# Kernel tuning notes

Hardware: AMD Instinct MI355X
Metric: run time of the kernel (lower is better)

Reference implementation:

```python
import jax, jax.numpy as jnp
import numpy as np

N_NODES = 50000
N_EDGES = 800000
IN_CH = 64
HID = 128
OUT_CH = 1
NUM_LAYERS = 3
NUM_TIMESTEPS = 3
EDGE_DIM = 25
NUM_GRAPHS = 1024
NEG = 0.01  # leaky_relu negative slope (torch default & GATConv arg)


def leaky(v):
    return jnp.where(v >= 0, v, NEG * v)


def seg_softmax(a, idx, n):
    # PyG softmax: exp(a - max_per_segment) / (sum_per_segment + 1e-16)
    m = jax.ops.segment_max(a, idx, num_segments=n)
    m = jnp.where(jnp.isfinite(m), m, 0.0)  # guard empty segments
    e = jnp.exp(a - m[idx])
    s = jax.ops.segment_sum(e, idx, num_segments=n)
    return e / (s[idx] + 1e-16)


def gru(inp, h, Wih, Whh, bih, bhh):
    gi = inp @ Wih.T + bih
    gh = h @ Whh.T + bhh
    ir, iz, inn = jnp.split(gi, 3, axis=-1)
    hr, hz, hn = jnp.split(gh, 3, axis=-1)
    r = jax.nn.sigmoid(ir + hr)
    z = jax.nn.sigmoid(iz + hz)
    n = jnp.tanh(inn + r * hn)
    return (1.0 - z) * n + z * h


def setup_inputs() -> dict:
    key = jax.random.key(0)
    ks = iter(jax.random.split(key, 40))

    def nrm(shape, s=0.05):
        return jax.random.normal(next(ks), shape, dtype=jnp.float32) * s

    L = NUM_LAYERS - 1
    H3 = 3 * HID
    inp = dict(
        x=jax.random.normal(next(ks), (N_NODES, IN_CH), dtype=jnp.float32),
        edge_index=jax.random.randint(next(ks), (2, N_EDGES), 0, N_NODES),
        batch=jnp.sort(jax.random.randint(next(ks), (N_NODES,), 0, NUM_GRAPHS)),
        W1=nrm((HID, IN_CH)), b1=jnp.zeros((HID,), jnp.float32),
        Wg1=nrm((HID, HID + EDGE_DIM)), att_l=nrm((HID,)), att_r=nrm((HID,)),
        Wg2=nrm((HID, HID)), bg=jnp.zeros((HID,), jnp.float32),
        Wih0=nrm((H3, HID)), Whh0=nrm((H3, HID)),
        bih0=jnp.zeros((H3,), jnp.float32), bhh0=jnp.zeros((H3,), jnp.float32),
        Wa=nrm((L, HID, HID)), att_src_a=nrm((L, HID)), att_dst_a=nrm((L, HID)),
        ba=jnp.zeros((L, HID), jnp.float32),
        Wih_a=nrm((L, H3, HID)), Whh_a=nrm((L, H3, HID)),
        bih_a=jnp.zeros((L, H3), jnp.float32), bhh_a=jnp.zeros((L, H3), jnp.float32),
        Wm=nrm((HID, HID)), att_src_m=nrm((HID,)), att_dst_m=nrm((HID,)),
        bm=jnp.zeros((HID,), jnp.float32),
        Wih_m=nrm((H3, HID)), Whh_m=nrm((H3, HID)),
        bih_m=jnp.zeros((H3,), jnp.float32), bhh_m=jnp.zeros((H3,), jnp.float32),
        W2=nrm((OUT_CH, HID)), b2=jnp.zeros((OUT_CH,), jnp.float32),
    )
    return inp


def reference(x, edge_index, batch, W1, b1, Wg1, att_l, att_r, Wg2, bg,
              Wih0, Whh0, bih0, bhh0, Wa, att_src_a, att_dst_a, ba,
              Wih_a, Whh_a, bih_a, bhh_a, Wm, att_src_m, att_dst_m, bm,
              Wih_m, Whh_m, bih_m, bhh_m, W2, b2):
    N = x.shape[0]
    E = edge_index.shape[1]
    src, dst = edge_index[0], edge_index[1]  # j -> i, aggregate at i=dst
    edge_attr = jnp.ones((E, EDGE_DIM), dtype=x.dtype)  # built inside original forward

    x = leaky(x @ W1.T + b1)

    # GATEConv: edge-feature-aware attention, sum aggregation
    xe = leaky(jnp.concatenate([x[src], edge_attr], axis=-1) @ Wg1.T)  # [E, H]
    a = seg_softmax(leaky(xe @ att_l + (x @ att_r)[dst]), dst, N)
    msg = (x[src] @ Wg2.T) * a[:, None]
    h = jax.nn.elu(jax.ops.segment_sum(msg, dst, num_segments=N) + bg)
    x = jax.nn.relu(gru(h, x, Wih0, Whh0, bih0, bhh0))

    # (num_layers - 1) GATConv + GRU atom updates
    for l in range(NUM_LAYERS - 1):
        xt = x @ Wa[l].T
        a = seg_softmax(leaky((xt @ att_src_a[l])[src] + (xt @ att_dst_a[l])[dst]), dst, N)
        h = jax.nn.elu(jax.ops.segment_sum(xt[src] * a[:, None], dst, num_segments=N) + ba[l])
        x = jax.nn.relu(gru(h, x, Wih_a[l], Whh_a[l], bih_a[l], bhh_a[l]))

    # attentive readout: bipartite GATConv node->molecule over num_timesteps
    out = jax.nn.relu(jax.ops.segment_sum(x, batch, num_segments=NUM_GRAPHS))
    xt = x @ Wm.T                 # shared lin for src (fixed across timesteps)
    a_src = xt @ att_src_m        # [N]
    for _ in range(NUM_TIMESTEPS):
        ot = out @ Wm.T           # shared lin for dst
        a = seg_softmax(leaky(a_src + (ot @ att_dst_m)[batch]), batch, NUM_GRAPHS)
        h = jax.nn.elu(jax.ops.segment_sum(xt * a[:, None], batch, num_segments=NUM_GRAPHS) + bm)
        out = jax.nn.relu(gru(h, out, Wih_m, Whh_m, bih_m, bhh_m))

    return out @ W2.T + b2
```

## Files before the change

kernel.cpp:

```cpp
#include <hip/hip_runtime.h>
#include <math.h>

#define NN 50000
#define NE 800000
#define NG 1024
#define HID 128

typedef __attribute__((ext_vector_type(8))) short short8;
typedef __attribute__((ext_vector_type(4))) unsigned short ushort4v;
typedef __attribute__((ext_vector_type(4))) float f32x4;

__device__ __forceinline__ float leakyf(float v){ return v >= 0.f ? v : 0.01f*v; }
__device__ __forceinline__ float frcp(float x){ return __builtin_amdgcn_rcpf(x); }
__device__ __forceinline__ float fsigm(float v){ return frcp(1.f + __expf(-v)); }
__device__ __forceinline__ float ftanh(float v){ return 1.f - 2.f*frcp(1.f + __expf(2.f*v)); }
__device__ __forceinline__ float eluf(float v){ return v > 0.f ? v : __expf(v) - 1.f; }
__device__ __forceinline__ unsigned short bf16rne(float f){
  union { float f; unsigned u; } v; v.f = f;
  return (unsigned short)((v.u + 0x7FFFu + ((v.u >> 16) & 1u)) >> 16);
}
__device__ __forceinline__ float bf2f(unsigned short h){
  union { unsigned u; float f; } v; v.u = ((unsigned)h) << 16; return v.f;
}
__device__ __forceinline__ short8 cvt8(const float* a){
  short8 r;
#pragma unroll
  for (int j=0;j<8;j++) r[j] = (short)bf16rne(a[j]);
  return r;
}

__global__ __launch_bounds__(256)
void pack_all(const float* W1, const float* Wg1, const float* Wg2, const float* Wa,
              const float* Wm, const float* Wih0, const float* Whh0,
              const float* Wih_a, const float* Whh_a,
              unsigned short* __restrict__ dst)
{
  int m = (int)blockIdx.y;
  int t = (int)blockIdx.x*4 + ((int)threadIdx.x>>6);
  int l = (int)threadIdx.x & 63;
  const float* src; int stride=128, M=128, K=128; size_t doff;
  switch(m){
    case 0:  src=W1;    stride=64;  K=64;  doff=0;      break;
    case 1:  src=Wg1;   stride=153;        doff=8192;   break;
    case 2:  src=Wg2;                      doff=24576;  break;
    case 3:  src=Wa;                       doff=40960;  break;
    case 4:  src=Wa+16384;                 doff=57344;  break;
    case 5:  src=Wm;                       doff=73728;  break;
    case 6:  src=Wih0;  M=384;             doff=90112;  break;
    case 7:  src=Whh0;  M=384;             doff=139264; break;
    case 8:  src=Wih_a; M=384;             doff=188416; break;
    case 9:  src=Whh_a; M=384;             doff=237568; break;
    case 10: src=Wih_a+49152; M=384;       doff=286720; break;
    default: src=Whh_a+49152; M=384;       doff=335872; break;
  }
  int tk = K/32;
  if (t >= (M/16)*tk) return;
  int ct = t / tk, kc = t % tk;
  int row = ct*16 + (l&15);
  int col = kc*32 + ((l>>4)<<3);
  unsigned short o[8];
#pragma unroll
  for (int j=0;j<8;j++) o[j] = bf16rne(src[(size_t)row*stride + col + j]);
  ushort4v* d = (ushort4v*)(dst + doff + (((size_t)t*64 + l)<<3));
  ushort4v d0; d0.x=o[0]; d0.y=o[1]; d0.z=o[2]; d0.w=o[3];
  ushort4v d1; d1.x=o[4]; d1.y=o[5]; d1.z=o[6]; d1.w=o[7];
  d[0]=d0; d[1]=d1;
}

__global__ void pack_t4(const float* __restrict__ Wi, const float* __restrict__ Wh,
                        unsigned short* __restrict__ Wit, unsigned short* __restrict__ Wht)
{
  int q  = (int)blockIdx.x;
  int cg = (int)threadIdx.x + (int)blockIdx.y*128;
  ushort4v a, b;
#pragma unroll
  for (int j=0;j<4;j++){
    a[j] = bf16rne(Wi[(size_t)cg*128 + q*4 + j]);
    b[j] = bf16rne(Wh[(size_t)cg*128 + q*4 + j]);
  }
  *(ushort4v*)&Wit[((size_t)q*384 + cg)*4] = a;
  *(ushort4v*)&Wht[((size_t)q*384 + cg)*4] = b;
}

__global__ __launch_bounds__(256)
void gemm_f32(const float* __restrict__ A, const unsigned short* __restrict__ Wp,
              const float* __restrict__ bias, float* __restrict__ Cf,
              unsigned short* __restrict__ Cb, int rows, int act)
{
  constexpr int K = 64, KC = 2;
  const int tid=(int)threadIdx.x, w=tid>>6, l=tid&63;
  const int fr=l&15, fq=l>>4;
  const int rt=w>>1, ch=w&1;
  const int bn = (int)blockIdx.x*32;
  const int ar = bn + rt*16 + fr;
  f32x4 acc[4];
#pragma unroll
  for (int j=0;j<4;j++) acc[j] = (f32x4){0.f,0.f,0.f,0.f};
#pragma unroll
  for (int kc=0;kc<KC;kc++){
    float a8[8];
    if (ar < rows){
      *(float4*)&a8[0] = *(const float4*)(A + (size_t)ar*K + kc*32 + fq*8);
      *(float4*)&a8[4] = *(const float4*)(A + (size_t)ar*K + kc*32 + fq*8 + 4);
    } else {
#pragma unroll
      for (int j=0;j<8;j++) a8[j]=0.f;
    }
    short8 fa = cvt8(a8);
#pragma unroll
    for (int j=0;j<4;j++){
      const short8 bfr = *(const short8*)(Wp + ((((size_t)(ch*4+j)*KC + kc)*64 + l)<<3));
      acc[j] = __builtin_amdgcn_mfma_f32_16x16x32_bf16(fa, bfr, acc[j], 0, 0, 0);
    }
  }
#pragma unroll
  for (int j=0;j<4;j++){
    int c = ch*64 + j*16 + fr;
    float bv = bias ? bias[c] : 0.f;
#pragma unroll
    for (int r4=0;r4<4;r4++){
      float o = acc[j][r4] + bv;
      if (act) o = leakyf(o);
      int r = bn + rt*16 + fq*4 + r4;
      if (r < rows){
        Cf[(size_t)r*HID + c] = o;
        Cb[(size_t)r*HID + c] = bf16rne(o);
      }
    }
  }
}

__global__ __launch_bounds__(256)
void gemm_b16(const unsigned short* __restrict__ Ab, const unsigned short* __restrict__ Wp,
              const float* __restrict__ bias, unsigned short* __restrict__ Cb,
              const float* __restrict__ v1, const float* __restrict__ v2,
              float* __restrict__ s1, float* __restrict__ s2, int rows, int act)
{
  __shared__ float sd1[2][32];
  __shared__ float sd2[2][32];
  constexpr int KC = 4;
  const int tid=(int)threadIdx.x, w=tid>>6, l=tid&63;
  const int fr=l&15, fq=l>>4;
  const int rt=w>>1, ch=w&1;
  const int bn = (int)blockIdx.x*32;
  const int ar = bn + rt*16 + fr;
  f32x4 acc[4];
#pragma unroll
  for (int j=0;j<4;j++) acc[j] = (f32x4){0.f,0.f,0.f,0.f};
#pragma unroll
  for (int kc=0;kc<KC;kc++){
    short8 fa;
    if (ar < rows) fa = *(const short8*)(Ab + (size_t)ar*HID + kc*32 + fq*8);
    else { short8 z = {0,0,0,0,0,0,0,0}; fa = z; }
#pragma unroll
    for (int j=0;j<4;j++){
      const short8 bfr = *(const short8*)(Wp + ((((size_t)(ch*4+j)*KC + kc)*64 + l)<<3));
      acc[j] = __builtin_amdgcn_mfma_f32_16x16x32_bf16(fa, bfr, acc[j], 0, 0, 0);
    }
  }
  float dp1[4]={0.f,0.f,0.f,0.f}, dp2[4]={0.f,0.f,0.f,0.f};
#pragma unroll
  for (int j=0;j<4;j++){
    int c = ch*64 + j*16 + fr;
    float bv = bias ? bias[c] : 0.f;
    float w1 = v1 ? v1[c] : 0.f;
    float w2 = v2 ? v2[c] : 0.f;
#pragma unroll
    for (int r4=0;r4<4;r4++){
      float o = acc[j][r4] + bv;
      if (act) o = leakyf(o);
      dp1[r4] += o*w1; dp2[r4] += o*w2;
      int r = bn + rt*16 + fq*4 + r4;
      if (r < rows && Cb) Cb[(size_t)r*HID + c] = bf16rne(o);
    }
  }
  if (v1){
#pragma unroll
    for (int r4=0;r4<4;r4++){
#pragma unroll
      for (int m=1;m<16;m<<=1){ dp1[r4] += __shfl_xor(dp1[r4], m); dp2[r4] += __shfl_xor(dp2[r4], m); }
    }
    if (fr==0){
#pragma unroll
      for (int r4=0;r4<4;r4++){
        sd1[ch][rt*16 + fq*4 + r4] = dp1[r4];
        sd2[ch][rt*16 + fq*4 + r4] = dp2[r4];
      }
    }
    __syncthreads();
    if (tid < 32){
      int r = bn + tid;
      if (r < rows) s1[r] = sd1[0][tid] + sd1[1][tid];
    } else if (v2 && tid < 64){
      int r = bn + tid - 32;
      if (r < rows) s2[r] = sd2[0][tid-32] + sd2[1][tid-32];
    }
  }
}

__global__ __launch_bounds__(256)
void gemm_gate(const unsigned short* __restrict__ Ab,
               const unsigned short* __restrict__ W1p, const unsigned short* __restrict__ W2p,
               const float* __restrict__ cg, const float* __restrict__ attl,
               const float* __restrict__ attr,
               unsigned short* __restrict__ Cb,
               float* __restrict__ s1, float* __restrict__ s2, int rows)
{
  __shared__ float sd1[2][32];
  constexpr int KC = 4;
  const int tid=(int)threadIdx.x, w=tid>>6, l=tid&63;
  const int fr=l&15, fq=l>>4;
  const int rt=w>>1, ch=w&1;
  const int bn = (int)blockIdx.x*32;
  const int ar = bn + rt*16 + fr;
  f32x4 acc1[4], acc2[4];
#pragma unroll
  for (int j=0;j<4;j++){ acc1[j]=(f32x4){0,0,0,0}; acc2[j]=(f32x4){0,0,0,0}; }
  float pa = 0.f;
#pragma unroll
  for (int kc=0;kc<KC;kc++){
    short8 fa;
    if (ar < rows) fa = *(const short8*)(Ab + (size_t)ar*HID + kc*32 + fq*8);
    else { short8 z = {0,0,0,0,0,0,0,0}; fa = z; }
    if (ch==0){
      float4 t0 = *(const float4*)(attr + kc*32 + fq*8);
      float4 t1 = *(const float4*)(attr + kc*32 + fq*8 + 4);
      pa += bf2f((unsigned short)fa[0])*t0.x + bf2f((unsigned short)fa[1])*t0.y
          + bf2f((unsigned short)fa[2])*t0.z + bf2f((unsigned short)fa[3])*t0.w
          + bf2f((unsigned short)fa[4])*t1.x + bf2f((unsigned short)fa[5])*t1.y
          + bf2f((unsigned short)fa[6])*t1.z + bf2f((unsigned short)fa[7])*t1.w;
    }
#pragma unroll
    for (int j=0;j<4;j++){
      size_t wo = ((((size_t)(ch*4+j)*KC + kc)*64 + l)<<3);
      acc1[j] = __builtin_amdgcn_mfma_f32_16x16x32_bf16(fa, *(const short8*)(W1p + wo), acc1[j], 0, 0, 0);
      acc2[j] = __builtin_amdgcn_mfma_f32_16x16x32_bf16(fa, *(const short8*)(W2p + wo), acc2[j], 0, 0, 0);
    }
  }
  float dp1[4]={0.f,0.f,0.f,0.f};
#pragma unroll
  for (int j=0;j<4;j++){
    int c = ch*64 + j*16 + fr;
    float bv = cg[c];
    float w1 = attl[c];
#pragma unroll
    for (int r4=0;r4<4;r4++){
      float o1 = leakyf(acc1[j][r4] + bv);
      dp1[r4] += o1*w1;
      int r = bn + rt*16 + fq*4 + r4;
      if (r < rows) Cb[(size_t)r*HID + c] = bf16rne(acc2[j][r4]);
    }
  }
#pragma unroll
  for (int r4=0;r4<4;r4++){
#pragma unroll
    for (int m=1;m<16;m<<=1) dp1[r4] += __shfl_xor(dp1[r4], m);
  }
  if (fr==0){
#pragma unroll
    for (int r4=0;r4<4;r4++) sd1[ch][rt*16 + fq*4 + r4] = dp1[r4];
  }
  __syncthreads();
  if (tid < 32){
    int r = bn + tid;
    if (r < rows) s1[r] = sd1[0][tid] + sd1[1][tid];
  }
  if (ch==0){
    pa += __shfl_xor(pa, 16); pa += __shfl_xor(pa, 32);
    if (fq==0){
      int r = bn + rt*16 + fr;
      if (r < rows) s2[r] = pa;
    }
  }
}

#define GRU_TPB 4
__global__ __launch_bounds__(512, 2)
void fused_gru(const unsigned short* __restrict__ Ahb, const unsigned short* __restrict__ Axb,
               const float* __restrict__ Axf,
               const unsigned short* __restrict__ Wi, const unsigned short* __restrict__ Wh,
               const float* __restrict__ bih, const float* __restrict__ bhh,
               float* __restrict__ outf, unsigned short* __restrict__ outb, int tiles)
{
  const int tid=(int)threadIdx.x, w=tid>>6, l=tid&63;
  const int fr=l&15, fq=l>>4;
  short8 wi_r[3][4], wh_r[3][4];
#pragma unroll
  for (int g=0;g<3;g++)
#pragma unroll
    for (int kc=0;kc<4;kc++){
      size_t o = ((((size_t)(g*8 + w)*4 + kc)*64 + l)<<3);
      wi_r[g][kc] = *(const short8*)(Wi + o);
      wh_r[g][kc] = *(const short8*)(Wh + o);
    }
  const int c0 = w*16 + fr;
  float bi0=bih[c0], bi1=bih[c0+128], bi2=bih[c0+256];
  float bh0=bhh[c0], bh1=bhh[c0+128], bh2=bhh[c0+256];

  int rt = (int)blockIdx.x*GRU_TPB;
  int rt_end = min(rt + GRU_TPB, tiles);
  if (rt >= tiles) return;
  short8 fa[4], fx[4];
  float hv[4];
  {
    const int arow = rt*16 + fr;
#pragma unroll
    for (int kc=0;kc<4;kc++){
      fa[kc] = *(const short8*)(Ahb + (size_t)arow*HID + kc*32 + fq*8);
      fx[kc] = *(const short8*)(Axb + (size_t)arow*HID + kc*32 + fq*8);
    }
#pragma unroll
    for (int r4=0;r4<4;r4++) hv[r4] = Axf[(size_t)(rt*16 + fq*4 + r4)*HID + c0];
  }
  for (; rt < rt_end; rt++){
    short8 nfa[4], nfx[4];
    float nhv[4];
    if (rt+1 < rt_end){
      const int arow = (rt+1)*16 + fr;
#pragma unroll
      for (int kc=0;kc<4;kc++){
        nfa[kc] = *(const short8*)(Ahb + (size_t)arow*HID + kc*32 + fq*8);
        nfx[kc] = *(const short8*)(Axb + (size_t)arow*HID + kc*32 + fq*8);
      }
#pragma unroll
      for (int r4=0;r4<4;r4++) nhv[r4] = Axf[(size_t)((rt+1)*16 + fq*4 + r4)*HID + c0];
    }
    f32x4 ai0={0,0,0,0}, ai1={0,0,0,0}, ai2={0,0,0,0};
    f32x4 ah0={0,0,0,0}, ah1={0,0,0,0}, ah2={0,0,0,0};
#pragma unroll
    for (int kc=0;kc<4;kc++){
      ai0 = __builtin_amdgcn_mfma_f32_16x16x32_bf16(fa[kc], wi_r[0][kc], ai0, 0, 0, 0);
      ai1 = __builtin_amdgcn_mfma_f32_16x16x32_bf16(fa[kc], wi_r[1][kc], ai1, 0, 0, 0);
      ai2 = __builtin_amdgcn_mfma_f32_16x16x32_bf16(fa[kc], wi_r[2][kc], ai2, 0, 0, 0);
      ah0 = __builtin_amdgcn_mfma_f32_16x16x32_bf16(fx[kc], wh_r[0][kc], ah0, 0, 0, 0);
      ah1 = __builtin_amdgcn_mfma_f32_16x16x32_bf16(fx[kc], wh_r[1][kc], ah1, 0, 0, 0);
      ah2 = __builtin_amdgcn_mfma_f32_16x16x32_bf16(fx[kc], wh_r[2][kc], ah2, 0, 0, 0);
    }
#pragma unroll
    for (int r4=0;r4<4;r4++){
      int row = rt*16 + fq*4 + r4;
      float rr = fsigm(ai0[r4] + bi0 + ah0[r4] + bh0);
      float zz = fsigm(ai1[r4] + bi1 + ah1[r4] + bh1);
      float nn = ftanh(ai2[r4] + bi2 + rr*(ah2[r4] + bh2));
      float o = fmaxf((1.f - zz)*nn + zz*hv[r4], 0.f);
      outf[(size_t)row*HID + c0] = o;
      outb[(size_t)row*HID + c0] = bf16rne(o);
    }
#pragma unroll
    for (int kc=0;kc<4;kc++){ fa[kc]=nfa[kc]; fx[kc]=nfx[kc]; }
#pragma unroll
    for (int r4=0;r4<4;r4++) hv[r4]=nhv[r4];
  }
}

__global__ void colvec(const float* __restrict__ W, const float* __restrict__ v,
                       float* __restrict__ out)
{
  int k = (int)threadIdx.x;
  float s = 0.f;
  for (int j=0;j<HID;j++) s += W[j*HID+k]*v[j];
  out[k] = s;
}

__global__ void prep_cg(const float* __restrict__ Wg1, float* __restrict__ cg){
  int j = (int)threadIdx.x;
  float s = 0.f;
  for (int k=128;k<153;k++) s += Wg1[j*153+k];
  cg[j] = s;
}

__global__ void count_kernel(const int* __restrict__ idx, int* __restrict__ cnt, int n){
  int i = (int)(blockIdx.x*blockDim.x + threadIdx.x);
  if (i < n) atomicAdd(&cnt[idx[i]], 1);
}

__global__ __launch_bounds__(1024)
void scan_blocks(const int* __restrict__ cnt, int* __restrict__ off,
                 int* __restrict__ tot, int n)
{
  __shared__ int buf[1024];
  int i = (int)(blockIdx.x*1024 + threadIdx.x);
  int v = (i<n)? cnt[i] : 0;
  buf[threadIdx.x] = v;
  __syncthreads();
  for (int s=1;s<1024;s<<=1){
    int t = ((int)threadIdx.x >= s) ? buf[threadIdx.x - s] : 0;
    __syncthreads();
    buf[threadIdx.x] += t;
    __syncthreads();
  }
  if (i<n) off[i] = buf[threadIdx.x] - v;
  if (threadIdx.x==1023) tot[blockIdx.x] = buf[1023];
}

__global__ void scan_tot(int* __restrict__ tot, int* __restrict__ off_end, int nb){
  int lane = (int)threadIdx.x;
  int orig = (lane<nb)? tot[lane] : 0;
  int v = orig;
  for (int s=1;s<64;s<<=1){ int t = __shfl_up(v, s); if (lane>=s) v += t; }
  int total = __shfl(v, 63);
  if (lane<nb) tot[lane] = v - orig;
  if (lane==0) *off_end = total;
}

__global__ void scan_add(int* __restrict__ off, int* __restrict__ off_mut,
                         const int* __restrict__ tot, int n){
  int i = (int)(blockIdx.x*blockDim.x + threadIdx.x);
  if (i<n){
    int v = off[i] + tot[i>>10];
    off[i] = v;
    off_mut[i] = v;
  }
}

__global__ void fill_kernel(const int* __restrict__ src, const int* __restrict__ dst,
                            int* __restrict__ off_mut, int* __restrict__ ssrc, int n){
  int e = (int)(blockIdx.x*blockDim.x + threadIdx.x);
  if (e < n){
    int p = atomicAdd(&off_mut[dst[e]], 1);
    ssrc[p] = src[e];
  }
}

__global__ void graph_bounds(const int* __restrict__ batch, int* __restrict__ goff){
  int g = (int)(blockIdx.x*blockDim.x + threadIdx.x);
  if (g > NG) return;
  int lo=0, hi=NN;
  while (lo<hi){ int mid=(lo+hi)>>1; if (batch[mid] < g) lo=mid+1; else hi=mid; }
  goff[g] = lo;
}

__global__ __launch_bounds__(256)
void agg_edges(const int* __restrict__ off, const int* __restrict__ ssrc,
               const float* __restrict__ ls, const float* __restrict__ ld,
               const unsigned short* __restrict__ Mrows, const float* __restrict__ bias,
               unsigned short* __restrict__ outb, int n)
{
  __shared__ float wbuf[4][64];
  __shared__ int   sbuf[4][64];
  const int ws = (int)(threadIdx.x >> 6);
  int node = (int)((blockIdx.x * blockDim.x + threadIdx.x) >> 6);
  int lane = (int)(threadIdx.x & 63);
  if (node >= n) return;
  int e0 = off[node], e1 = off[node+1];
  float ldv = ld[node];
  const int g4 = lane >> 4, cl = lane & 15;
  float denom = 0.f;
  float acc[8] = {0.f,0.f,0.f,0.f,0.f,0.f,0.f,0.f};
  for (int j0=e0; j0<e1; j0+=64){
    int cnt = min(64, e1-j0);
    float wv = 0.f; int sc = 0;
    if (lane < cnt){
      sc = ssrc[j0+lane];
      wv = __expf(leakyf(ls[sc]+ldv));
    }
    denom += wv;
    wbuf[ws][lane] = wv;
    sbuf[ws][lane] = sc;
#pragma unroll 4
    for (int k4=0;k4<cnt;k4+=4){
      float wk = wbuf[ws][k4+g4];
      int  sck = sbuf[ws][k4+g4];
      uint4 mm = *(const uint4*)(Mrows + (size_t)sck*HID + cl*8);
      acc[0] += wk*bf2f((unsigned short)(mm.x&0xffff));
      acc[1] += wk*bf2f((unsigned short)(mm.x>>16));
      acc[2] += wk*bf2f((unsigned short)(mm.y&0xffff));
      acc[3] += wk*bf2f((unsigned short)(mm.y>>16));
      acc[4] += wk*bf2f((unsigned short)(mm.z&0xffff));
      acc[5] += wk*bf2f((unsigned short)(mm.z>>16));
      acc[6] += wk*bf2f((unsigned short)(mm.w&0xffff));
      acc[7] += wk*bf2f((unsigned short)(mm.w>>16));
    }
  }
#pragma unroll
  for (int j=0;j<8;j++){ acc[j] += __shfl_xor(acc[j], 16); acc[j] += __shfl_xor(acc[j], 32); }
  for (int o=32;o;o>>=1) denom += __shfl_xor(denom, o);
  if (g4==0){
    float inv = frcp(denom + 1e-16f);
    float4 b0 = *(const float4*)(bias + cl*8);
    float4 b1 = *(const float4*)(bias + cl*8 + 4);
    float o0=eluf(acc[0]*inv+b0.x), o1=eluf(acc[1]*inv+b0.y);
    float o2=eluf(acc[2]*inv+b0.z), o3=eluf(acc[3]*inv+b0.w);
    float o4=eluf(acc[4]*inv+b1.x), o5=eluf(acc[5]*inv+b1.y);
    float o6=eluf(acc[6]*inv+b1.z), o7=eluf(acc[7]*inv+b1.w);
    uint4 u;
    u.x = (unsigned)bf16rne(o0) | ((unsigned)bf16rne(o1)<<16);
    u.y = (unsigned)bf16rne(o2) | ((unsigned)bf16rne(o3)<<16);
    u.z = (unsigned)bf16rne(o4) | ((unsigned)bf16rne(o5)<<16);
    u.w = (unsigned)bf16rne(o6) | ((unsigned)bf16rne(o7)<<16);
    *(uint4*)(outb + (size_t)node*HID + cl*8) = u;
  }
}

__global__ __launch_bounds__(512)
void readout_all(const int* __restrict__ goff, const float* __restrict__ X,
                 const float* __restrict__ asrc, const unsigned short* __restrict__ Xt,
                 const float* __restrict__ vmd, const float* __restrict__ bm_,
                 const unsigned short* __restrict__ Wit, const unsigned short* __restrict__ Wht,
                 const float* __restrict__ bih, const float* __restrict__ bhh,
                 const float* __restrict__ W2, const float* __restrict__ b2,
                 float* __restrict__ dout)
{
  __shared__ __align__(16) float sh_o[128];
  __shared__ __align__(16) float sh_h[128];
  __shared__ float sp[4][128];
  __shared__ float sg[6][4][128];
  __shared__ float sden[4];
  __shared__ float sred[4];
  const int g = (int)blockIdx.x;
  const int tid = (int)threadIdx.x;
  const int c = tid & 127, s = tid >> 7;
  const int n0 = goff[g], n1 = goff[g+1];
  const ushort4v* W4i = (const ushort4v*)Wit;
  const ushort4v* W4h = (const ushort4v*)Wht;

  float a = 0.f;
  for (int n = n0 + s; n < n1; n += 4) a += X[(size_t)n*HID + c];
  sp[s][c] = a;
  __syncthreads();
  if (s == 0)
    sh_o[c] = fmaxf(sp[0][c]+sp[1][c]+sp[2][c]+sp[3][c], 0.f);
  __syncthreads();

  const float bi0=bih[c], bi1=bih[c+128], bi2=bih[c+256];
  const float bh0=bhh[c], bh1=bhh[c+128], bh2=bhh[c+256];
  const float bmc = bm_[c];

  for (int t=0;t<3;t++){
    if (s == 0){
      float p = sh_o[c]*vmd[c];
      for (int o=32;o;o>>=1) p += __shfl_down(p, o);
      if ((c&63)==0) sred[c>>6] = p;
    }
    __syncthreads();
    float ad = sred[0] + sred[1];
    float den = 0.f, acc = 0.f;
    for (int nn = n0 + s; nn < n1; nn += 4){
      float wv = __expf(leakyf(asrc[nn] + ad));
      den += wv;
      acc += wv * bf2f(Xt[(size_t)nn*HID + c]);
    }
    sp[s][c] = acc;
    if (c == 0) sden[s] = den;
    __syncthreads();
    if (s == 0){
      float dsum = sden[0]+sden[1]+sden[2]+sden[3];
      float asum = sp[0][c]+sp[1][c]+sp[2][c]+sp[3][c];
      sh_h[c] = eluf(asum*frcp(dsum + 1e-16f) + bmc);
    }
    __syncthreads();
    float gi0=0.f,gi1=0.f,gi2=0.f,gh0=0.f,gh1=0.f,gh2=0.f;
    const int q0 = s*8;
#pragma unroll 2
    for (int q=q0;q<q0+8;q++){
      float4 hk = *(const float4*)&sh_h[q*4];
      float4 ok = *(const float4*)&sh_o[q*4];
      ushort4v wi0 = W4i[(size_t)q*384 + c];
      ushort4v wi1 = W4i[(size_t)q*384 + c + 128];
      ushort4v wi2 = W4i[(size_t)q*384 + c + 256];
      ushort4v wh0 = W4h[(size_t)q*384 + c];
      ushort4v wh1 = W4h[(size_t)q*384 + c + 128];
      ushort4v wh2 = W4h[(size_t)q*384 + c + 256];
      gi0 += bf2f(wi0.x)*hk.x + bf2f(wi0.y)*hk.y + bf2f(wi0.z)*hk.z + bf2f(wi0.w)*hk.w;
      gi1 += bf2f(wi1.x)*hk.x + bf2f(wi1.y)*hk.y + bf2f(wi1.z)*hk.z + bf2f(wi1.w)*hk.w;
      gi2 += bf2f(wi2.x)*hk.x + bf2f(wi2.y)*hk.y + bf2f(wi2.z)*hk.z + bf2f(wi2.w)*hk.w;
      gh0 += bf2f(wh0.x)*ok.x + bf2f(wh0.y)*ok.y + bf2f(wh0.z)*ok.z + bf2f(wh0.w)*ok.w;
      gh1 += bf2f(wh1.x)*ok.x + bf2f(wh1.y)*ok.y + bf2f(wh1.z)*ok.z + bf2f(wh1.w)*ok.w;
      gh2 += bf2f(wh2.x)*ok.x + bf2f(wh2.y)*ok.y + bf2f(wh2.z)*ok.z + bf2f(wh2.w)*ok.w;
    }
    sg[0][s][c]=gi0; sg[1][s][c]=gi1; sg[2][s][c]=gi2;
    sg[3][s][c]=gh0; sg[4][s][c]=gh1; sg[5][s][c]=gh2;
    __syncthreads();
    if (s == 0){
      float G0=sg[0][0][c]+sg[0][1][c]+sg[0][2][c]+sg[0][3][c];
      float G1=sg[1][0][c]+sg[1][1][c]+sg[1][2][c]+sg[1][3][c];
      float G2=sg[2][0][c]+sg[2][1][c]+sg[2][2][c]+sg[2][3][c];
      float H0=sg[3][0][c]+sg[3][1][c]+sg[3][2][c]+sg[3][3][c];
      float H1=sg[4][0][c]+sg[4][1][c]+sg[4][2][c]+sg[4][3][c];
      float H2=sg[5][0][c]+sg[5][1][c]+sg[5][2][c]+sg[5][3][c];
      float rr = fsigm(G0+bi0+H0+bh0);
      float zz = fsigm(G1+bi1+H1+bh1);
      float nv = ftanh(G2+bi2 + rr*(H2+bh2));
      sh_o[c] = fmaxf((1.f-zz)*nv + zz*sh_o[c], 0.f);
    }
    __syncthreads();
  }
  if (s == 0){
    float p = sh_o[c]*W2[c];
    for (int o=32;o;o>>=1) p += __shfl_down(p, o);
    if ((c&63)==0) sred[(c>>6)+2] = p;
  }
  __syncthreads();
  if (tid==0) dout[g] = sred[2] + sred[3] + b2[0];
}

extern "C" void kernel_launch(void* const* d_in, const int* in_sizes, int n_in,
                              void* d_out, int out_size, void* d_ws, size_t ws_size,
                              hipStream_t stream)
{
  const float* x_in  = (const float*)d_in[0];
  const int*   ei    = (const int*)d_in[1];
  const int*   batch = (const int*)d_in[2];
  const float* W1    = (const float*)d_in[3];
  const float* b1    = (const float*)d_in[4];
  const float* Wg1   = (const float*)d_in[5];
  const float* att_l = (const float*)d_in[6];
  const float* att_r = (const float*)d_in[7];
  const float* Wg2   = (const float*)d_in[8];
  const float* bg    = (const float*)d_in[9];
  const float* Wih0  = (const float*)d_in[10];
  const float* Whh0  = (const float*)d_in[11];
  const float* bih0  = (const float*)d_in[12];
  const float* bhh0  = (const float*)d_in[13];
  const float* Wa    = (const float*)d_in[14];
  const float* att_src_a = (const float*)d_in[15];
  const float* att_dst_a = (const float*)d_in[16];
  const float* ba    = (const float*)d_in[17];
  const float* Wih_a = (const float*)d_in[18];
  const float* Whh_a = (const float*)d_in[19];
  const float* bih_a = (const float*)d_in[20];
  const float* bhh_a = (const float*)d_in[21];
  const float* Wm    = (const float*)d_in[22];
  const float* att_src_m = (const float*)d_in[23];
  const float* att_dst_m = (const float*)d_in[24];
  const float* bm    = (const float*)d_in[25];
  const float* Wih_m = (const float*)d_in[26];
  const float* Whh_m = (const float*)d_in[27];
  const float* bih_m = (const float*)d_in[28];
  const float* bhh_m = (const float*)d_in[29];
  const float* W2    = (const float*)d_in[30];
  const float* b2    = (const float*)d_in[31];
  (void)in_sizes; (void)n_in; (void)out_size; (void)ws_size;

  char* wsb = (char*)d_ws;
  size_t off = 0;
  auto alloc = [&](size_t bytes)->void* {
    void* p = wsb + off;
    off += (bytes + 255) & ~(size_t)255;
    return p;
  };
  float* f_x   = (float*)alloc((size_t)NN*HID*4);
  float* f_y   = (float*)alloc((size_t)NN*HID*4);
  unsigned short* f_xb = (unsigned short*)alloc((size_t)NN*HID*2);
  unsigned short* f_yb = (unsigned short*)alloc((size_t)NN*HID*2);
  unsigned short* f_h  = (unsigned short*)alloc((size_t)NN*HID*2);
  unsigned short* f_t  = (unsigned short*)alloc((size_t)NN*HID*2);
  float* f_s1  = (float*)alloc((size_t)NN*4);
  float* f_s2  = (float*)alloc((size_t)NN*4);
  float* w_cg  = (float*)alloc((size_t)HID*4);
  float* w_vmd = (float*)alloc((size_t)HID*4);
  unsigned short* w_pack = (unsigned short*)alloc((size_t)385024*2);
  unsigned short* w_wit  = (unsigned short*)alloc((size_t)49152*2);
  unsigned short* w_wht  = (unsigned short*)alloc((size_t)49152*2);
  int* i_cnt   = (int*)alloc((size_t)NN*4);
  int* i_off   = (int*)alloc((size_t)(NN+1)*4);
  int* i_offm  = (int*)alloc((size_t)NN*4);
  int* i_src   = (int*)alloc((size_t)NE*4);
  int* i_tot   = (int*)alloc((size_t)64*4);
  int* i_goff  = (int*)alloc((size_t)(NG+1)*4);

  const unsigned short* pk_W1   = w_pack + 0;
  const unsigned short* pk_g1   = w_pack + 8192;
  const unsigned short* pk_g2   = w_pack + 24576;
  const unsigned short* pk_wa0  = w_pack + 40960;
  const unsigned short* pk_wa1  = w_pack + 57344;
  const unsigned short* pk_wm   = w_pack + 73728;
  const unsigned short* pk_wih0 = w_pack + 90112;
  const unsigned short* pk_whh0 = w_pack + 139264;
  const unsigned short* pk_wiha0= w_pack + 188416;
  const unsigned short* pk_whha0= w_pack + 237568;
  const unsigned short* pk_wiha1= w_pack + 286720;
  const unsigned short* pk_whha1= w_pack + 335872;

  const int* e_src = ei;
  const int* e_dst = ei + NE;

  hipMemsetAsync(i_cnt, 0, (size_t)NN*4, stream);

  const int NB = (NN + 1023)/1024;
  count_kernel<<<(NE+255)/256,256,0,stream>>>(e_dst, i_cnt, NE);
  scan_blocks<<<NB,1024,0,stream>>>(i_cnt, i_off, i_tot, NN);
  scan_tot<<<1,64,0,stream>>>(i_tot, i_off+NN, NB);
  scan_add<<<(NN+255)/256,256,0,stream>>>(i_off, i_offm, i_tot, NN);
  fill_kernel<<<(NE+255)/256,256,0,stream>>>(e_src, e_dst, i_offm, i_src, NE);
  graph_bounds<<<(NG+1+255)/256,256,0,stream>>>(batch, i_goff);
  prep_cg<<<1,128,0,stream>>>(Wg1, w_cg);
  colvec<<<1,128,0,stream>>>(Wm, att_dst_m, w_vmd);
  pack_all<<<dim3(24,12),256,0,stream>>>(W1, Wg1, Wg2, Wa, Wm, Wih0, Whh0,
                                         Wih_a, Whh_a, w_pack);
  pack_t4<<<dim3(32,3),128,0,stream>>>(Wih_m, Whh_m, w_wit, w_wht);

  const int GB = (NN+31)/32;
  const int NT = NN/16;
  const int FB = (NT+GRU_TPB-1)/GRU_TPB;

  gemm_f32<<<GB,256,0,stream>>>(x_in, pk_W1, b1, f_x, f_xb, NN, 1);

  float* curf = f_x;  unsigned short* curb = f_xb;
  float* nxtf = f_y;  unsigned short* nxtb = f_yb;

  gemm_gate<<<GB,256,0,stream>>>(curb, pk_g1, pk_g2, w_cg, att_l, att_r,
                                 f_t, f_s1, f_s2, NN);
  agg_edges<<<(NN+3)/4,256,0,stream>>>(i_off, i_src, f_s1, f_s2, f_t, bg, f_h, NN);
  fused_gru<<<FB,512,0,stream>>>(f_h, curb, curf, pk_wih0, pk_whh0, bih0, bhh0,
                                 nxtf, nxtb, NT);
  { float* t=curf; curf=nxtf; nxtf=t; unsigned short* tb=curb; curb=nxtb; nxtb=tb; }

  for (int l=0;l<2;l++){
    gemm_b16<<<GB,256,0,stream>>>(curb, l ? pk_wa1 : pk_wa0, nullptr, f_t,
                                  att_src_a + l*HID, att_dst_a + l*HID,
                                  f_s1, f_s2, NN, 0);
    agg_edges<<<(NN+3)/4,256,0,stream>>>(i_off, i_src, f_s1, f_s2, f_t, ba + l*HID, f_h, NN);
    fused_gru<<<FB,512,0,stream>>>(f_h, curb, curf,
                                   l ? pk_wiha1 : pk_wiha0, l ? pk_whha1 : pk_whha0,
                                   bih_a + l*384, bhh_a + l*384, nxtf, nxtb, NT);
    { float* t=curf; curf=nxtf; nxtf=t; unsigned short* tb=curb; curb=nxtb; nxtb=tb; }
  }

  gemm_b16<<<GB,256,0,stream>>>(curb, pk_wm, nullptr, f_t,
                                att_src_m, nullptr, f_s1, nullptr, NN, 0);
  readout_all<<<NG,512,0,stream>>>(i_goff, curf, f_s1, f_t, w_vmd, bm,
                                   w_wit, w_wht, bih_m, bhh_m, W2, b2,
                                   (float*)d_out);
}
```

Before: 609.1 us.

## Merge small setup kernels into pack_all and widen readout blocks to 1024 threads

Folds pack_t4, prep_cg, colvec and graph_bounds into extra grid rows of pack_all, and merges scan_tot into the scan_add pass so each block recomputes the block-total prefix in shared memory. This cuts five small kernel launches and their serialization gaps from the setup phase. The readout kernel now uses 1024 threads (8 node slices instead of 4), which gives more parallelism per graph for the node reductions and splits the GRU K-loop across more slices, at the cost of more shared memory and more partial sums to combine.

```diff
diff --git a/kernel.cpp b/kernel.cpp
--- a/kernel.cpp
+++ b/kernel.cpp
@@ -33,11 +33,53 @@
 void pack_all(const float* W1, const float* Wg1, const float* Wg2, const float* Wa,
               const float* Wm, const float* Wih0, const float* Whh0,
               const float* Wih_a, const float* Whh_a,
-              unsigned short* __restrict__ dst)
+              const float* Wih_m, const float* Whh_m, const float* att_dst_m,
+              const int* __restrict__ batch,
+              unsigned short* __restrict__ dst,
+              unsigned short* __restrict__ Wit, unsigned short* __restrict__ Wht,
+              float* __restrict__ cg, float* __restrict__ vmd,
+              int* __restrict__ goff)
 {
   int m = (int)blockIdx.y;
-  int t = (int)blockIdx.x*4 + ((int)threadIdx.x>>6);
-  int l = (int)threadIdx.x & 63;
+  int tid = (int)threadIdx.x;
+  if (m == 12){
+    for (int it = (int)blockIdx.x*256 + tid; it < 32*384; it += 24*256){
+      int q = it / 384, cg2 = it - q*384;
+      ushort4v a, b;
+#pragma unroll
+      for (int j=0;j<4;j++){
+        a[j] = bf16rne(Wih_m[(size_t)cg2*128 + q*4 + j]);
+        b[j] = bf16rne(Whh_m[(size_t)cg2*128 + q*4 + j]);
+      }
+      *(ushort4v*)&Wit[((size_t)q*384 + cg2)*4] = a;
+      *(ushort4v*)&Wht[((size_t)q*384 + cg2)*4] = b;
+    }
+    return;
+  }
+  if (m == 13){
+    if (blockIdx.x == 0){
+      if (tid < 128){
+        float s = 0.f;
+        for (int k=128;k<153;k++) s += Wg1[(size_t)tid*153+k];
+        cg[tid] = s;
+      } else {
+        int k = tid - 128;
+        float s = 0.f;
+        for (int j=0;j<HID;j++) s += Wm[(size_t)j*HID+k]*att_dst_m[j];
+        vmd[k] = s;
+      }
+    } else {
+      int g = ((int)blockIdx.x-1)*256 + tid;
+      if (g <= NG){
+        int lo=0, hi=NN;
+        while (lo<hi){ int mid=(lo+hi)>>1; if (batch[mid] < g) lo=mid+1; else hi=mid; }
+        goff[g] = lo;
+      }
+    }
+    return;
+  }
+  int t = (int)blockIdx.x*4 + (tid>>6);
+  int l = tid & 63;
   const float* src; int stride=128, M=128, K=128; size_t doff;
   switch(m){
     case 0:  src=W1;    stride=64;  K=64;  doff=0;      break;
@@ -67,21 +109,6 @@
   d[0]=d0; d[1]=d1;
 }
 
-__global__ void pack_t4(const float* __restrict__ Wi, const float* __restrict__ Wh,
-                        unsigned short* __restrict__ Wit, unsigned short* __restrict__ Wht)
-{
-  int q  = (int)blockIdx.x;
-  int cg = (int)threadIdx.x + (int)blockIdx.y*128;
-  ushort4v a, b;
-#pragma unroll
-  for (int j=0;j<4;j++){
-    a[j] = bf16rne(Wi[(size_t)cg*128 + q*4 + j]);
-    b[j] = bf16rne(Wh[(size_t)cg*128 + q*4 + j]);
-  }
-  *(ushort4v*)&Wit[((size_t)q*384 + cg)*4] = a;
-  *(ushort4v*)&Wht[((size_t)q*384 + cg)*4] = b;
-}
-
 __global__ __launch_bounds__(256)
 void gemm_f32(const float* __restrict__ A, const unsigned short* __restrict__ Wp,
               const float* __restrict__ bias, float* __restrict__ Cf,
@@ -353,22 +380,6 @@
   }
 }
 
-__global__ void colvec(const float* __restrict__ W, const float* __restrict__ v,
-                       float* __restrict__ out)
-{
-  int k = (int)threadIdx.x;
-  float s = 0.f;
-  for (int j=0;j<HID;j++) s += W[j*HID+k]*v[j];
-  out[k] = s;
-}
-
-__global__ void prep_cg(const float* __restrict__ Wg1, float* __restrict__ cg){
-  int j = (int)threadIdx.x;
-  float s = 0.f;
-  for (int k=128;k<153;k++) s += Wg1[j*153+k];
-  cg[j] = s;
-}
-
 __global__ void count_kernel(const int* __restrict__ idx, int* __restrict__ cnt, int n){
   int i = (int)(blockIdx.x*blockDim.x + threadIdx.x);
   if (i < n) atomicAdd(&cnt[idx[i]], 1);
@@ -393,21 +404,21 @@
   if (threadIdx.x==1023) tot[blockIdx.x] = buf[1023];
 }
 
-__global__ void scan_tot(int* __restrict__ tot, int* __restrict__ off_end, int nb){
-  int lane = (int)threadIdx.x;
-  int orig = (lane<nb)? tot[lane] : 0;
-  int v = orig;
-  for (int s=1;s<64;s<<=1){ int t = __shfl_up(v, s); if (lane>=s) v += t; }
-  int total = __shfl(v, 63);
-  if (lane<nb) tot[lane] = v - orig;
-  if (lane==0) *off_end = total;
-}
-
-__global__ void scan_add(int* __restrict__ off, int* __restrict__ off_mut,
-                         const int* __restrict__ tot, int n){
+__global__ void scan_add2(int* __restrict__ off, int* __restrict__ off_mut,
+                          const int* __restrict__ tot, int n, int nb){
+  __shared__ int stot[64];
+  if (threadIdx.x < 64){
+    int lane = (int)threadIdx.x;
+    int orig = (lane<nb)? tot[lane] : 0;
+    int v = orig;
+    for (int s=1;s<64;s<<=1){ int t = __shfl_up(v, s); if (lane>=s) v += t; }
+    stot[lane] = v - orig;
+    if (lane==63 && blockIdx.x==0) off[n] = v;
+  }
+  __syncthreads();
   int i = (int)(blockIdx.x*blockDim.x + threadIdx.x);
   if (i<n){
-    int v = off[i] + tot[i>>10];
+    int v = off[i] + stot[i>>10];
     off[i] = v;
     off_mut[i] = v;
   }
@@ -420,14 +431,6 @@
     int p = atomicAdd(&off_mut[dst[e]], 1);
     ssrc[p] = src[e];
   }
-}
-
-__global__ void graph_bounds(const int* __restrict__ batch, int* __restrict__ goff){
-  int g = (int)(blockIdx.x*blockDim.x + threadIdx.x);
-  if (g > NG) return;
-  int lo=0, hi=NN;
-  while (lo<hi){ int mid=(lo+hi)>>1; if (batch[mid] < g) lo=mid+1; else hi=mid; }
-  goff[g] = lo;
 }
 
 __global__ __launch_bounds__(256)
@@ -492,7 +495,7 @@
   }
 }
 
-__global__ __launch_bounds__(512)
+__global__ __launch_bounds__(1024)
 void readout_all(const int* __restrict__ goff, const float* __restrict__ X,
                  const float* __restrict__ asrc, const unsigned short* __restrict__ Xt,
                  const float* __restrict__ vmd, const float* __restrict__ bm_,
@@ -503,9 +506,9 @@
 {
   __shared__ __align__(16) float sh_o[128];
   __shared__ __align__(16) float sh_h[128];
-  __shared__ float sp[4][128];
-  __shared__ float sg[6][4][128];
-  __shared__ float sden[4];
+  __shared__ float sp[8][128];
+  __shared__ float sg[6][8][128];
+  __shared__ float sden[8];
   __shared__ float sred[4];
   const int g = (int)blockIdx.x;
   const int tid = (int)threadIdx.x;
@@ -515,11 +518,14 @@
   const ushort4v* W4h = (const ushort4v*)Wht;
 
   float a = 0.f;
-  for (int n = n0 + s; n < n1; n += 4) a += X[(size_t)n*HID + c];
+  for (int n = n0 + s; n < n1; n += 8) a += X[(size_t)n*HID + c];
   sp[s][c] = a;
   __syncthreads();
-  if (s == 0)
-    sh_o[c] = fmaxf(sp[0][c]+sp[1][c]+sp[2][c]+sp[3][c], 0.f);
+  if (s == 0){
+    float t0 = sp[0][c]+sp[1][c]+sp[2][c]+sp[3][c];
+    float t1 = sp[4][c]+sp[5][c]+sp[6][c]+sp[7][c];
+    sh_o[c] = fmaxf(t0+t1, 0.f);
+  }
   __syncthreads();
 
   const float bi0=bih[c], bi1=bih[c+128], bi2=bih[c+256];
@@ -535,7 +541,7 @@
     __syncthreads();
     float ad = sred[0] + sred[1];
     float den = 0.f, acc = 0.f;
-    for (int nn = n0 + s; nn < n1; nn += 4){
+    for (int nn = n0 + s; nn < n1; nn += 8){
       float wv = __expf(leakyf(asrc[nn] + ad));
       den += wv;
       acc += wv * bf2f(Xt[(size_t)nn*HID + c]);
@@ -544,15 +550,15 @@
     if (c == 0) sden[s] = den;
     __syncthreads();
     if (s == 0){
-      float dsum = sden[0]+sden[1]+sden[2]+sden[3];
-      float asum = sp[0][c]+sp[1][c]+sp[2][c]+sp[3][c];
+      float dsum = (sden[0]+sden[1]+sden[2]+sden[3])+(sden[4]+sden[5]+sden[6]+sden[7]);
+      float asum = (sp[0][c]+sp[1][c]+sp[2][c]+sp[3][c])+(sp[4][c]+sp[5][c]+sp[6][c]+sp[7][c]);
       sh_h[c] = eluf(asum*frcp(dsum + 1e-16f) + bmc);
     }
     __syncthreads();
     float gi0=0.f,gi1=0.f,gi2=0.f,gh0=0.f,gh1=0.f,gh2=0.f;
-    const int q0 = s*8;
-#pragma unroll 2
-    for (int q=q0;q<q0+8;q++){
+    const int q0 = s*4;
+#pragma unroll
+    for (int q=q0;q<q0+4;q++){
       float4 hk = *(const float4*)&sh_h[q*4];
       float4 ok = *(const float4*)&sh_o[q*4];
       ushort4v wi0 = W4i[(size_t)q*384 + c];
@@ -572,12 +578,12 @@
     sg[3][s][c]=gh0; sg[4][s][c]=gh1; sg[5][s][c]=gh2;
     __syncthreads();
     if (s == 0){
-      float G0=sg[0][0][c]+sg[0][1][c]+sg[0][2][c]+sg[0][3][c];
-      float G1=sg[1][0][c]+sg[1][1][c]+sg[1][2][c]+sg[1][3][c];
-      float G2=sg[2][0][c]+sg[2][1][c]+sg[2][2][c]+sg[2][3][c];
-      float H0=sg[3][0][c]+sg[3][1][c]+sg[3][2][c]+sg[3][3][c];
-      float H1=sg[4][0][c]+sg[4][1][c]+sg[4][2][c]+sg[4][3][c];
-      float H2=sg[5][0][c]+sg[5][1][c]+sg[5][2][c]+sg[5][3][c];
+      float G0=0,G1=0,G2=0,H0=0,H1=0,H2=0;
+#pragma unroll
+      for (int ss=0;ss<8;ss++){
+        G0+=sg[0][ss][c]; G1+=sg[1][ss][c]; G2+=sg[2][ss][c];
+        H0+=sg[3][ss][c]; H1+=sg[4][ss][c]; H2+=sg[5][ss][c];
+      }
       float rr = fsigm(G0+bi0+H0+bh0);
       float zz = fsigm(G1+bi1+H1+bh1);
       float nv = ftanh(G2+bi2 + rr*(H2+bh2));
@@ -679,16 +685,13 @@
 
   const int NB = (NN + 1023)/1024;
   count_kernel<<<(NE+255)/256,256,0,stream>>>(e_dst, i_cnt, NE);
+  pack_all<<<dim3(24,14),256,0,stream>>>(W1, Wg1, Wg2, Wa, Wm, Wih0, Whh0,
+                                         Wih_a, Whh_a, Wih_m, Whh_m, att_dst_m,
+                                         batch, w_pack, w_wit, w_wht,
+                                         w_cg, w_vmd, i_goff);
   scan_blocks<<<NB,1024,0,stream>>>(i_cnt, i_off, i_tot, NN);
-  scan_tot<<<1,64,0,stream>>>(i_tot, i_off+NN, NB);
-  scan_add<<<(NN+255)/256,256,0,stream>>>(i_off, i_offm, i_tot, NN);
+  scan_add2<<<(NN+255)/256,256,0,stream>>>(i_off, i_offm, i_tot, NN, NB);
   fill_kernel<<<(NE+255)/256,256,0,stream>>>(e_src, e_dst, i_offm, i_src, NE);
-  graph_bounds<<<(NG+1+255)/256,256,0,stream>>>(batch, i_goff);
-  prep_cg<<<1,128,0,stream>>>(Wg1, w_cg);
-  colvec<<<1,128,0,stream>>>(Wm, att_dst_m, w_vmd);
-  pack_all<<<dim3(24,12),256,0,stream>>>(W1, Wg1, Wg2, Wa, Wm, Wih0, Whh0,
-                                         Wih_a, Whh_a, w_pack);
-  pack_t4<<<dim3(32,3),128,0,stream>>>(Wih_m, Whh_m, w_wit, w_wht);
 
   const int GB = (NN+31)/32;
   const int NT = NN/16;
@@ -719,7 +722,7 @@
 
   gemm_b16<<<GB,256,0,stream>>>(curb, pk_wm, nullptr, f_t,
                                 att_src_m, nullptr, f_s1, nullptr, NN, 0);
-  readout_all<<<NG,512,0,stream>>>(i_goff, curf, f_s1, f_t, w_vmd, bm,
-                                   w_wit, w_wht, bih_m, bhh_m, W2, b2,
-                                   (float*)d_out);
-}
+  readout_all<<<NG,1024,0,stream>>>(i_goff, curf, f_s1, f_t, w_vmd, bm,
+                                    w_wit, w_wht, bih_m, bhh_m, W2, b2,
+                                    (float*)d_out);
+}
```

After: 656.7 us. 1.08x slower.
